# Performance work log

Measured on AMD Instinct MI355X. Metric: run time of the kernel, lower is better.

Reference implementation:

```python
import jax, jax.numpy as jnp
import numpy as np
import math

EMBED = 1024
HEADS = 16
HEAD_DIM = EMBED // HEADS
B, S = 4, 2048
FF = 4 * EMBED
EPS = 1e-5


def _layernorm(x, g, b):
    mu = jnp.mean(x, axis=-1, keepdims=True)
    var = jnp.mean(jnp.square(x - mu), axis=-1, keepdims=True)
    return (x - mu) * jax.lax.rsqrt(var + EPS) * g + b


def setup_inputs() -> dict:
    key = jax.random.key(0)
    ks = jax.random.split(key, 12)
    sd_e = 1.0 / math.sqrt(EMBED)
    sd_ff = 1.0 / math.sqrt(FF)
    return {
        "x": jax.random.normal(ks[0], (B, S, EMBED), jnp.float32),
        # attention weights stored [in, out] (transposed torch Linear)
        "Wq": jax.random.normal(ks[1], (EMBED, EMBED), jnp.float32) * sd_e,
        "bq": jnp.zeros((EMBED,), jnp.float32),
        "Wk": jax.random.normal(ks[2], (EMBED, EMBED), jnp.float32) * sd_e,
        "bk": jnp.zeros((EMBED,), jnp.float32),
        "Wv": jax.random.normal(ks[3], (EMBED, EMBED), jnp.float32) * sd_e,
        "bv": jnp.zeros((EMBED,), jnp.float32),
        "Wo": jax.random.normal(ks[4], (EMBED, EMBED), jnp.float32) * sd_e,
        "bo": jnp.zeros((EMBED,), jnp.float32),
        "g1": jnp.ones((EMBED,), jnp.float32),
        "beta1": jnp.zeros((EMBED,), jnp.float32),
        "g2": jnp.ones((EMBED,), jnp.float32),
        "beta2": jnp.zeros((EMBED,), jnp.float32),
        "W1": jax.random.normal(ks[5], (EMBED, FF), jnp.float32) * sd_e,
        "b1": jnp.zeros((FF,), jnp.float32),
        "W2": jax.random.normal(ks[6], (FF, EMBED), jnp.float32) * sd_ff,
        "b2": jnp.zeros((EMBED,), jnp.float32),
    }


def reference(x, Wq, bq, Wk, bk, Wv, bv, Wo, bo, g1, beta1, g2, beta2, W1, b1, W2, b2):
    b, s, _ = x.shape
    # --- pre-LN causal self-attention (dropout in eval = identity) ---
    h = _layernorm(x, g1, beta1)
    q = (h @ Wq + bq).reshape(b, s, HEADS, HEAD_DIM)
    k = (h @ Wk + bk).reshape(b, s, HEADS, HEAD_DIM)
    v = (h @ Wv + bv).reshape(b, s, HEADS, HEAD_DIM)
    scores = jnp.einsum("bqhd,bkhd->bhqk", q, k) / math.sqrt(HEAD_DIM)
    causal = jnp.tril(jnp.ones((s, s), bool))
    scores = jnp.where(causal, scores, jnp.float32(-1e8))
    attn = jax.nn.softmax(scores, axis=-1)
    y = jnp.einsum("bhqk,bkhd->bqhd", attn, v).reshape(b, s, EMBED)
    x = x + (y @ Wo + bo)
    # --- GELU MLP (exact erf gelu, torch default) ---
    h2 = _layernorm(x, g2, beta2)
    ff = jax.nn.gelu(h2 @ W1 + b1, approximate=False) @ W2 + b2
    return x + ff
```

## Files before the change

### kernel.cpp

```cpp
#include <hip/hip_runtime.h>
#include <hip/hip_bf16.h>
#include <stdint.h>
#include <math.h>

#define SEQ 2048
#define NTOK 8192
#define EMB 1024
#define NH 16
#define HD 64
#define FFD 4096

using us = unsigned short;
using b8 = __attribute__((ext_vector_type(8))) __bf16;
using f4 = __attribute__((ext_vector_type(4))) float;

__device__ __forceinline__ us f2b(float f) {
  union { float f; uint32_t u; } v; v.f = f;
  uint32_t u = v.u;
  return (us)((u + 0x7fffu + ((u >> 16) & 1u)) >> 16);
}

__device__ __forceinline__ uint32_t pkbf(float a, float b) {
  union { float f; uint32_t u; } x, y; x.f = a; y.f = b;
  return ((x.u + 0x8000u) >> 16) | ((y.u + 0x8000u) & 0xFFFF0000u);
}

__device__ __forceinline__ void async16(void* lds, const void* g) {
  __builtin_amdgcn_global_load_lds(
      (__attribute__((address_space(1))) void*)(uintptr_t)g,
      (__attribute__((address_space(3))) void*)(uintptr_t)lds, 16, 0, 0);
}

#define FENCED_BARRIER() do { asm volatile("" ::: "memory"); \
  __builtin_amdgcn_s_barrier(); asm volatile("" ::: "memory"); } while (0)

__device__ __forceinline__ float gelu_f(float x) {
  const float z = -2.30211416f * x * (1.f + 0.044715f * x * x);
  return x / (1.f + __builtin_amdgcn_exp2f(z));
}

__global__ __launch_bounds__(256)
void transpose_cast(const float* __restrict__ in, us* __restrict__ out, int R, int C) {
  __shared__ float tile[32][33];
  const int bc = blockIdx.x * 32, br = blockIdx.y * 32;
  const int tx = threadIdx.x & 31, ty = threadIdx.x >> 5;
#pragma unroll
  for (int i = 0; i < 32; i += 8)
    tile[ty + i][tx] = in[(size_t)(br + ty + i) * C + bc + tx];
  __syncthreads();
#pragma unroll
  for (int i = 0; i < 32; i += 8)
    out[(size_t)(bc + ty + i) * R + br + tx] = f2b(tile[tx][ty + i]);
}

__global__ void pack_bias(const float* __restrict__ bq, const float* __restrict__ bk,
                          const float* __restrict__ bv, float* __restrict__ o) {
  int i = blockIdx.x * 256 + threadIdx.x;
  o[i] = (i < 1024) ? bq[i] : (i < 2048 ? bk[i - 1024] : bv[i - 2048]);
}

__global__ __launch_bounds__(256)
void ln_kernel(const float* __restrict__ x, const float* __restrict__ g,
               const float* __restrict__ be, us* __restrict__ out) {
  __shared__ float red[8];
  const int row = blockIdx.x, t = threadIdx.x;
  const float4 v = ((const float4*)(x + (size_t)row * EMB))[t];
  float s = v.x + v.y + v.z + v.w;
  float s2 = v.x * v.x + v.y * v.y + v.z * v.z + v.w * v.w;
#pragma unroll
  for (int o = 32; o; o >>= 1) { s += __shfl_down(s, o, 64); s2 += __shfl_down(s2, o, 64); }
  if ((t & 63) == 0) { red[(t >> 6) * 2] = s; red[(t >> 6) * 2 + 1] = s2; }
  __syncthreads();
  const float ts = red[0] + red[2] + red[4] + red[6];
  const float ts2 = red[1] + red[3] + red[5] + red[7];
  const float mu = ts * (1.f / 1024.f);
  const float rs = rsqrtf(ts2 * (1.f / 1024.f) - mu * mu + 1e-5f);
  const float4 gv = ((const float4*)g)[t];
  const float4 bv = ((const float4*)be)[t];
  ushort4 o4;
  o4.x = f2b((v.x - mu) * rs * gv.x + bv.x);
  o4.y = f2b((v.y - mu) * rs * gv.y + bv.y);
  o4.z = f2b((v.z - mu) * rs * gv.z + bv.z);
  o4.w = f2b((v.w - mu) * rs * gv.w + bv.w);
  ((ushort4*)(out + (size_t)row * EMB))[t] = o4;
}

__global__ __launch_bounds__(512, 2)
void gemm256(const us* __restrict__ A, const us* __restrict__ Bt,
             const float* __restrict__ bias, us* __restrict__ outB,
             int N, int K, int gelu, int gy) {
  __shared__ us As[2][256 * 64];
  __shared__ us Bs[2][256 * 64];

  int bid = blockIdx.x;
  const int cpx = (int)gridDim.x >> 3;
  bid = (bid & 7) * cpx + (bid >> 3);
  const int bx = bid / gy, by = bid - bx * gy;
  const int row0 = bx * 256, col0 = by * 256;

  const int tid = threadIdx.x, w = tid >> 6, lane = tid & 63;
  const int wm = w >> 2, wn = w & 3;
  const int quad = lane >> 4, l15 = lane & 15;
  const int xr = l15 & 7;

  const int u0 = w * 2, u1 = u0 + 1;
  const int ar0 = ((u0 & 7) << 3) + ((u0 >> 3) << 7);
  const int ar1 = ((u1 & 7) << 3) + ((u1 >> 3) << 7);
  const int br0 = ((u0 & 3) << 3) + ((u0 >> 2) << 6);
  const int br1 = ((u1 & 3) << 3) + ((u1 >> 2) << 6);
  const int lrow = lane >> 3;
  const int loct = ((lane & 7) ^ lrow) << 3;
  const us* Ag0 = A + (size_t)(row0 + ar0 + lrow) * K + loct;
  const us* Ag1 = A + (size_t)(row0 + ar1 + lrow) * K + loct;
  const us* Bg0 = Bt + (size_t)(col0 + br0 + lrow) * K + loct;
  const us* Bg1 = Bt + (size_t)(col0 + br1 + lrow) * K + loct;
  const int NT = K >> 6;

  const f4 zf = {0.f, 0.f, 0.f, 0.f};
  f4 acc[8][4];
#pragma unroll
  for (int i = 0; i < 8; i++)
#pragma unroll
    for (int j = 0; j < 4; j++) acc[i][j] = zf;

  auto stgA = [&](int buf, int t, int mh) {
    const size_t go = (size_t)(mh << 6) * K + ((size_t)t << 6);
    async16(&As[buf][(ar0 + (mh << 6)) << 6], Ag0 + go);
    async16(&As[buf][(ar1 + (mh << 6)) << 6], Ag1 + go);
  };
  auto stgB = [&](int buf, int t, int nh) {
    const size_t go = (size_t)(nh << 5) * K + ((size_t)t << 6);
    async16(&Bs[buf][(br0 + (nh << 5)) << 6], Bg0 + go);
    async16(&Bs[buf][(br1 + (nh << 5)) << 6], Bg1 + go);
  };

  stgA(0, 0, 0); stgB(0, 0, 0); stgB(0, 0, 1); stgA(0, 0, 1);
  stgA(1, 1, 0); stgB(1, 1, 0); stgB(1, 1, 1);
  asm volatile("s_waitcnt vmcnt(6)" ::: "memory");
  FENCED_BARRIER();

  for (int t = 0; t < NT; t++) {
    const int cur = t & 1, nxt = cur ^ 1;
    const us* __restrict__ as = As[cur];
    const us* __restrict__ bs = Bs[cur];
    b8 af[2][4], bf0[2][2], bf1[2][2];

#pragma unroll
    for (int s = 0; s < 2; s++) {
      const int po = (((s << 2) + quad) ^ xr) << 3;
#pragma unroll
      for (int mi = 0; mi < 4; mi++)
        af[s][mi] = *(const b8*)&as[(wm * 128 + mi * 16 + l15) * 64 + po];
#pragma unroll
      for (int nf = 0; nf < 2; nf++)
        bf0[s][nf] = *(const b8*)&bs[(wn * 64 + nf * 16 + l15) * 64 + po];
    }
    if (t + 1 < NT) stgA(nxt, t + 1, 1);
    FENCED_BARRIER();
    asm volatile("s_waitcnt lgkmcnt(0)" ::: "memory");
    __builtin_amdgcn_s_setprio(1);
#pragma unroll
    for (int s = 0; s < 2; s++)
#pragma unroll
      for (int mi = 0; mi < 4; mi++)
#pragma unroll
        for (int nf = 0; nf < 2; nf++)
          acc[mi][nf] = __builtin_amdgcn_mfma_f32_16x16x32_bf16(af[s][mi], bf0[s][nf], acc[mi][nf], 0, 0, 0);
    __builtin_amdgcn_s_setprio(0);
    FENCED_BARRIER();

#pragma unroll
    for (int s = 0; s < 2; s++) {
      const int po = (((s << 2) + quad) ^ xr) << 3;
#pragma unroll
      for (int nf = 0; nf < 2; nf++)
        bf1[s][nf] = *(const b8*)&bs[(wn * 64 + 32 + nf * 16 + l15) * 64 + po];
    }
    if (t + 2 < NT) stgA(cur, t + 2, 0);
    FENCED_BARRIER();
    asm volatile("s_waitcnt lgkmcnt(0)" ::: "memory");
    __builtin_amdgcn_s_setprio(1);
#pragma unroll
    for (int s = 0; s < 2; s++)
#pragma unroll
      for (int mi = 0; mi < 4; mi++)
#pragma unroll
        for (int nf = 0; nf < 2; nf++)
          acc[mi][2 + nf] = __builtin_amdgcn_mfma_f32_16x16x32_bf16(af[s][mi], bf1[s][nf], acc[mi][2 + nf], 0, 0, 0);
    __builtin_amdgcn_s_setprio(0);
    FENCED_BARRIER();

#pragma unroll
    for (int s = 0; s < 2; s++) {
      const int po = (((s << 2) + quad) ^ xr) << 3;
#pragma unroll
      for (int mi = 0; mi < 4; mi++)
        af[s][mi] = *(const b8*)&as[(wm * 128 + 64 + mi * 16 + l15) * 64 + po];
    }
    if (t + 2 < NT) stgB(cur, t + 2, 0);
    FENCED_BARRIER();
    asm volatile("s_waitcnt lgkmcnt(0)" ::: "memory");
    __builtin_amdgcn_s_setprio(1);
#pragma unroll
    for (int s = 0; s < 2; s++)
#pragma unroll
      for (int mi = 0; mi < 4; mi++)
#pragma unroll
        for (int nf = 0; nf < 2; nf++)
          acc[4 + mi][nf] = __builtin_amdgcn_mfma_f32_16x16x32_bf16(af[s][mi], bf0[s][nf], acc[4 + mi][nf], 0, 0, 0);
    __builtin_amdgcn_s_setprio(0);
    FENCED_BARRIER();

    if (t + 2 < NT) {
      stgB(cur, t + 2, 1);
      asm volatile("s_waitcnt vmcnt(6)" ::: "memory");
    } else {
      asm volatile("s_waitcnt vmcnt(0)" ::: "memory");
    }
    FENCED_BARRIER();
    __builtin_amdgcn_s_setprio(1);
#pragma unroll
    for (int s = 0; s < 2; s++)
#pragma unroll
      for (int mi = 0; mi < 4; mi++)
#pragma unroll
        for (int nf = 0; nf < 2; nf++)
          acc[4 + mi][2 + nf] = __builtin_amdgcn_mfma_f32_16x16x32_bf16(af[s][mi], bf1[s][nf], acc[4 + mi][2 + nf], 0, 0, 0);
    __builtin_amdgcn_s_setprio(0);
    FENCED_BARRIER();
  }

#pragma unroll
  for (int mi8 = 0; mi8 < 8; mi8++)
#pragma unroll
    for (int nf = 0; nf < 4; nf++) {
      const int gcol = col0 + wn * 64 + nf * 16 + l15;
      const float bc = bias[gcol];
#pragma unroll
      for (int r = 0; r < 4; r++) {
        const int grow = row0 + wm * 128 + mi8 * 16 + quad * 4 + r;
        float v = acc[mi8][nf][r] + bc;
        if (gelu) v = gelu_f(v);
        outB[(size_t)grow * N + gcol] = f2b(v);
      }
    }
}

__global__ __launch_bounds__(512, 2)
void gemm128(const us* __restrict__ A, const us* __restrict__ Bt,
             const float* __restrict__ bias, const float* __restrict__ resid,
             float* __restrict__ outF, int N, int K, int gy) {
  __shared__ us As[2][128 * 64];
  __shared__ us Bs[2][256 * 64];

  int bid = blockIdx.x;
  const int cpx = (int)gridDim.x >> 3;
  bid = (bid & 7) * cpx + (bid >> 3);
  const int bx = bid / gy, by = bid - bx * gy;
  const int row0 = bx * 128, col0 = by * 256;

  const int tid = threadIdx.x, w = tid >> 6, lane = tid & 63;
  const int wm = w >> 2, wn = w & 3;
  const int quad = lane >> 4, l15 = lane & 15;
  const int xr = l15 & 7;

  const int u0 = w * 2, u1 = u0 + 1;
  const int aR0 = u0 << 3, aR1 = u1 << 3;
  const int bR0 = ((u0 & 3) << 3) + ((u0 >> 2) << 6);
  const int bR1 = ((u1 & 3) << 3) + ((u1 >> 2) << 6);
  const int lrow = lane >> 3;
  const int loct = ((lane & 7) ^ lrow) << 3;
  const us* Ag0 = A + (size_t)(row0 + aR0 + lrow) * K + loct;
  const us* Ag1 = A + (size_t)(row0 + aR1 + lrow) * K + loct;
  const us* Bg0 = Bt + (size_t)(col0 + bR0 + lrow) * K + loct;
  const us* Bg1 = Bt + (size_t)(col0 + bR1 + lrow) * K + loct;
  const int NT = K >> 6;

  const f4 zf = {0.f, 0.f, 0.f, 0.f};
  f4 acc[4][4];
#pragma unroll
  for (int i = 0; i < 4; i++)
#pragma unroll
    for (int j = 0; j < 4; j++) acc[i][j] = zf;

  auto stgA = [&](int buf, int t) {
    const size_t go = (size_t)t << 6;
    async16(&As[buf][aR0 << 6], Ag0 + go);
    async16(&As[buf][aR1 << 6], Ag1 + go);
  };
  auto stgB = [&](int buf, int t, int nh) {
    const size_t go = (size_t)(nh << 5) * K + ((size_t)t << 6);
    async16(&Bs[buf][(bR0 + (nh << 5)) << 6], Bg0 + go);
    async16(&Bs[buf][(bR1 + (nh << 5)) << 6], Bg1 + go);
  };

  stgA(0, 0); stgB(0, 0, 0); stgB(0, 0, 1);
  stgA(1, 1); stgB(1, 1, 0);
  asm volatile("s_waitcnt vmcnt(6)" ::: "memory");
  FENCED_BARRIER();

  for (int t = 0; t < NT; t++) {
    const int cur = t & 1, nxt = cur ^ 1;
    const us* __restrict__ as = As[cur];
    const us* __restrict__ bs = Bs[cur];
    b8 af[2][4], bf0[2][2], bf1[2][2];

#pragma unroll
    for (int s = 0; s < 2; s++) {
      const int po = (((s << 2) + quad) ^ xr) << 3;
#pragma unroll
      for (int mi = 0; mi < 4; mi++)
        af[s][mi] = *(const b8*)&as[(wm * 64 + mi * 16 + l15) * 64 + po];
#pragma unroll
      for (int nf = 0; nf < 2; nf++)
        bf0[s][nf] = *(const b8*)&bs[(wn * 64 + nf * 16 + l15) * 64 + po];
    }
    if (t + 1 < NT) {
      stgB(nxt, t + 1, 1);
      asm volatile("s_waitcnt vmcnt(6)" ::: "memory");
    } else {
      asm volatile("s_waitcnt vmcnt(0)" ::: "memory");
    }
    FENCED_BARRIER();
    asm volatile("s_waitcnt lgkmcnt(0)" ::: "memory");
    __builtin_amdgcn_s_setprio(1);
#pragma unroll
    for (int s = 0; s < 2; s++)
#pragma unroll
      for (int mi = 0; mi < 4; mi++)
#pragma unroll
        for (int nf = 0; nf < 2; nf++)
          acc[mi][nf] = __builtin_amdgcn_mfma_f32_16x16x32_bf16(af[s][mi], bf0[s][nf], acc[mi][nf], 0, 0, 0);
    __builtin_amdgcn_s_setprio(0);
    FENCED_BARRIER();

#pragma unroll
    for (int s = 0; s < 2; s++) {
      const int po = (((s << 2) + quad) ^ xr) << 3;
#pragma unroll
      for (int nf = 0; nf < 2; nf++)
        bf1[s][nf] = *(const b8*)&bs[(wn * 64 + 32 + nf * 16 + l15) * 64 + po];
    }
    if (t + 2 < NT) {
      stgA(cur, t + 2); stgB(cur, t + 2, 0);
      asm volatile("s_waitcnt vmcnt(6)" ::: "memory");
    } else {
      asm volatile("s_waitcnt vmcnt(2)" ::: "memory");
    }
    FENCED_BARRIER();
    asm volatile("s_waitcnt lgkmcnt(0)" ::: "memory");
    __builtin_amdgcn_s_setprio(1);
#pragma unroll
    for (int s = 0; s < 2; s++)
#pragma unroll
      for (int mi = 0; mi < 4; mi++)
#pragma unroll
        for (int nf = 0; nf < 2; nf++)
          acc[mi][2 + nf] = __builtin_amdgcn_mfma_f32_16x16x32_bf16(af[s][mi], bf1[s][nf], acc[mi][2 + nf], 0, 0, 0);
    __builtin_amdgcn_s_setprio(0);
    FENCED_BARRIER();
  }

#pragma unroll
  for (int mi = 0; mi < 4; mi++)
#pragma unroll
    for (int nf = 0; nf < 4; nf++) {
      const int gcol = col0 + wn * 64 + nf * 16 + l15;
      const float bc = bias[gcol];
#pragma unroll
      for (int r = 0; r < 4; r++) {
        const int grow = row0 + wm * 64 + mi * 16 + quad * 4 + r;
        outF[(size_t)grow * N + gcol] = acc[mi][nf][r] + bc + resid[(size_t)grow * N + gcol];
      }
    }
}

__global__ __launch_bounds__(256, 3)
void attn(const us* __restrict__ qkv, us* __restrict__ y) {
  static const signed char QTM[16] = {15,14,13,12, 10,11,8,9, 5,4,7,6, 0,1,2,3};
  const int bx = blockIdx.x;
  const int bh = bx & 63;
  const int qt = QTM[(bx >> 6) & 15];
  const int bb = bh >> 4, h = bh & 15;
  const int tid = threadIdx.x;
  const int wave = tid >> 6, lane = tid & 63;
  const int quad = lane >> 4, l15 = lane & 15;

  __shared__ us Ks[128 * 64];
  __shared__ us Vt[64 * 132];

  const size_t base = (size_t)bb * SEQ * 3072;
  const int q0 = qt * 128;

  b8 bqf[2][2];
#pragma unroll
  for (int qg = 0; qg < 2; qg++) {
    const us* qp = qkv + base + (size_t)(q0 + wave * 32 + qg * 16 + l15) * 3072 + h * 64 + quad * 8;
    bqf[qg][0] = *(const b8*)qp;
    bqf[qg][1] = *(const b8*)(qp + 32);
  }

  const f4 zf = {0.f, 0.f, 0.f, 0.f};
  f4 o[2][4];
  float mrow[2], lrow[2];
#pragma unroll
  for (int qg = 0; qg < 2; qg++) {
    mrow[qg] = -3.0e38f; lrow[qg] = 0.f;
#pragma unroll
    for (int dg = 0; dg < 4; dg++) o[qg][dg] = zf;
  }

  const int klr = lane >> 3, klc = lane & 7;
  const us* kgbase = qkv + base + (size_t)(wave * 32 + klr) * 3072 + 1024 + h * 64 + ((klc ^ klr) << 3);
  const us* vgbase = qkv + base + (size_t)(2 * lane) * 3072 + 2048 + h * 64 + wave * 8;

  const float sm_scale = 0.125f * 1.44269504088896340736f;

  for (int kt = 0; kt <= qt; kt++) {
    const size_t koff = (size_t)kt * 128 * 3072;
#pragma unroll
    for (int op = 0; op < 4; op++)
      async16(&Ks[(wave * 32 + op * 8) * 64], kgbase + koff + (size_t)op * 8 * 3072);
    {
      union { float4 f; us u[8]; } v0, v1, v2, v3;
      v0.f = *(const float4*)(vgbase + koff);
      v1.f = *(const float4*)(vgbase + koff + 3072);
      v2.f = *(const float4*)(vgbase + koff + 32);
      v3.f = *(const float4*)(vgbase + koff + 3072 + 32);
#pragma unroll
      for (int j = 0; j < 8; j++) {
        *(uint32_t*)&Vt[(wave * 8 + j) * 132 + 2 * lane] =
            (uint32_t)v0.u[j] | ((uint32_t)v1.u[j] << 16);
        *(uint32_t*)&Vt[(32 + wave * 8 + j) * 132 + 2 * lane] =
            (uint32_t)v2.u[j] | ((uint32_t)v3.u[j] << 16);
      }
    }
    __syncthreads();

    f4 sacc[2][8];
#pragma unroll
    for (int c = 0; c < 8; c++) {
      const int krow = (c * 16 + l15) * 64;
      const int sw = l15 & 7;
      const b8 ak0 = *(const b8*)&Ks[krow + ((quad ^ sw) << 3)];
      const b8 ak1 = *(const b8*)&Ks[krow + (((quad ^ 4) ^ sw) << 3)];
#pragma unroll
      for (int qg = 0; qg < 2; qg++) {
        f4 s = __builtin_amdgcn_mfma_f32_16x16x32_bf16(ak0, bqf[qg][0], zf, 0, 0, 0);
        sacc[qg][c] = __builtin_amdgcn_mfma_f32_16x16x32_bf16(ak1, bqf[qg][1], s, 0, 0, 0);
      }
    }

    uint32_t pf[2][16];
    float alpha[2];
#pragma unroll
    for (int qg = 0; qg < 2; qg++) {
      const int q_in = wave * 32 + qg * 16 + l15;
#pragma unroll
      for (int c = 0; c < 8; c++)
#pragma unroll
        for (int r = 0; r < 4; r++) {
          float v = sacc[qg][c][r] * sm_scale;
          if (kt == qt && (c * 16 + quad * 4 + r) > q_in) v = -3.0e38f;
          sacc[qg][c][r] = v;
        }
      float mx = sacc[qg][0][0];
#pragma unroll
      for (int c = 0; c < 8; c++)
#pragma unroll
        for (int r = 0; r < 4; r++) mx = fmaxf(mx, sacc[qg][c][r]);
      mx = fmaxf(mx, __shfl_xor(mx, 16, 64));
      mx = fmaxf(mx, __shfl_xor(mx, 32, 64));
      const float mnew = fmaxf(mrow[qg], mx);
      alpha[qg] = __builtin_amdgcn_exp2f(mrow[qg] - mnew);
      mrow[qg] = mnew;
      float rs = 0.f;
#pragma unroll
      for (int c = 0; c < 8; c++) {
        const float p0 = __builtin_amdgcn_exp2f(sacc[qg][c][0] - mnew);
        const float p1 = __builtin_amdgcn_exp2f(sacc[qg][c][1] - mnew);
        const float p2 = __builtin_amdgcn_exp2f(sacc[qg][c][2] - mnew);
        const float p3 = __builtin_amdgcn_exp2f(sacc[qg][c][3] - mnew);
        rs += (p0 + p1) + (p2 + p3);
        pf[qg][c * 2] = pkbf(p0, p1);
        pf[qg][c * 2 + 1] = pkbf(p2, p3);
      }
      rs += __shfl_xor(rs, 16, 64);
      rs += __shfl_xor(rs, 32, 64);
      lrow[qg] = lrow[qg] * alpha[qg] + rs;
#pragma unroll
      for (int r = 0; r < 4; r++) {
        const float ar = __shfl(alpha[qg], quad * 4 + r, 64);
#pragma unroll
        for (int dg = 0; dg < 4; dg++) o[qg][dg][r] *= ar;
      }
    }

#pragma unroll
    for (int c = 0; c < 8; c++) {
      union { uint32_t w[4]; b8 v; } af0, af1;
      af0.w[0] = pf[0][c * 2]; af0.w[1] = pf[0][c * 2 + 1]; af0.w[2] = 0u; af0.w[3] = 0u;
      af1.w[0] = pf[1][c * 2]; af1.w[1] = pf[1][c * 2 + 1]; af1.w[2] = 0u; af1.w[3] = 0u;
#pragma unroll
      for (int dg = 0; dg < 4; dg++) {
        const uint2 vd = *(const uint2*)&Vt[(dg * 16 + l15) * 132 + c * 16 + quad * 4];
        union { uint32_t w[4]; b8 v; } vb;
        vb.w[0] = vd.x; vb.w[1] = vd.y; vb.w[2] = 0u; vb.w[3] = 0u;
        o[0][dg] = __builtin_amdgcn_mfma_f32_16x16x32_bf16(af0.v, vb.v, o[0][dg], 0, 0, 0);
        o[1][dg] = __builtin_amdgcn_mfma_f32_16x16x32_bf16(af1.v, vb.v, o[1][dg], 0, 0, 0);
      }
    }
    __syncthreads();
  }

#pragma unroll
  for (int qg = 0; qg < 2; qg++) {
    float lr[4];
#pragma unroll
    for (int r = 0; r < 4; r++) lr[r] = __shfl(lrow[qg], quad * 4 + r, 64);
#pragma unroll
    for (int dg = 0; dg < 4; dg++)
#pragma unroll
      for (int r = 0; r < 4; r++) {
        const int gq = q0 + wave * 32 + qg * 16 + quad * 4 + r;
        y[(size_t)(bb * SEQ + gq) * EMB + h * 64 + dg * 16 + l15] = f2b(o[qg][dg][r] / lr[r]);
      }
  }
}

extern "C" void kernel_launch(void* const* d_in, const int* in_sizes, int n_in,
                              void* d_out, int out_size, void* d_ws, size_t ws_size,
                              hipStream_t stream) {
  const float* x = (const float*)d_in[0];
  const float* Wq = (const float*)d_in[1];
  const float* bq = (const float*)d_in[2];
  const float* Wk = (const float*)d_in[3];
  const float* bk = (const float*)d_in[4];
  const float* Wv = (const float*)d_in[5];
  const float* bv = (const float*)d_in[6];
  const float* Wo = (const float*)d_in[7];
  const float* bo = (const float*)d_in[8];
  const float* g1 = (const float*)d_in[9];
  const float* be1 = (const float*)d_in[10];
  const float* g2 = (const float*)d_in[11];
  const float* be2 = (const float*)d_in[12];
  const float* W1 = (const float*)d_in[13];
  const float* b1 = (const float*)d_in[14];
  const float* W2 = (const float*)d_in[15];
  const float* b2 = (const float*)d_in[16];
  float* out = (float*)d_out;

  char* ws = (char*)d_ws;
  const size_t MB = 1024ull * 1024ull;
  us* WqkvT = (us*)(ws + 0);
  us* WoT   = (us*)(ws + 6 * MB);
  us* W1T   = (us*)(ws + 8 * MB);
  us* W2T   = (us*)(ws + 16 * MB);
  us* hbuf  = (us*)(ws + 24 * MB);
  us* qkvb  = (us*)(ws + 40 * MB);
  us* ybuf  = (us*)(ws + 88 * MB);
  float* x1 = (float*)(ws + 104 * MB);
  us* h2    = (us*)(ws + 136 * MB);
  us* ff1   = (us*)(ws + 24 * MB);
  float* bqkv = (float*)(ws + 152 * MB);

  transpose_cast<<<dim3(32, 32), 256, 0, stream>>>(Wq, WqkvT, 1024, 1024);
  transpose_cast<<<dim3(32, 32), 256, 0, stream>>>(Wk, WqkvT + 1024 * 1024, 1024, 1024);
  transpose_cast<<<dim3(32, 32), 256, 0, stream>>>(Wv, WqkvT + 2 * 1024 * 1024, 1024, 1024);
  transpose_cast<<<dim3(32, 32), 256, 0, stream>>>(Wo, WoT, 1024, 1024);
  transpose_cast<<<dim3(128, 32), 256, 0, stream>>>(W1, W1T, 1024, 4096);
  transpose_cast<<<dim3(32, 128), 256, 0, stream>>>(W2, W2T, 4096, 1024);
  pack_bias<<<12, 256, 0, stream>>>(bq, bk, bv, bqkv);

  ln_kernel<<<NTOK, 256, 0, stream>>>(x, g1, be1, hbuf);
  gemm256<<<dim3(384), 512, 0, stream>>>(hbuf, WqkvT, bqkv, qkvb, 3072, 1024, 0, 12);
  attn<<<1024, 256, 0, stream>>>(qkvb, ybuf);
  gemm128<<<dim3(256), 512, 0, stream>>>(ybuf, WoT, bo, x, x1, 1024, 1024, 4);
  ln_kernel<<<NTOK, 256, 0, stream>>>(x1, g2, be2, h2);
  gemm256<<<dim3(512), 512, 0, stream>>>(h2, W1T, b1, ff1, 4096, 1024, 1, 16);
  gemm128<<<dim3(256), 512, 0, stream>>>(ff1, W2T, b2, x1, out, 1024, 4096, 4);
}
```

Baseline: 540.8 us.

## Fold softmax scale into Wq, prefetch V, lazy rescale in attention

Folds the 1/sqrt(d)·log2(e) softmax scale into the Wq weights and q bias during the weight cast, so the per-element scale multiply leaves the attention loop. The next V tile is now prefetched into registers while the current tile is computed, with explicit waitcnt and barriers. Online-softmax rescaling is skipped unless the running max grows by more than 8 (in log2 units), and s_setprio is raised around the MFMA sections. Occupancy hint goes from 3 to 4 blocks per CU, which constrains registers even though the prefetch needs more of them. The lazy rescale allows unnormalized values up to 2^8, and scaling Wq before the bf16 cast changes rounding slightly.

After: 628.1 us. 1.16x slower.

```diff
diff --git a/kernel.cpp b/kernel.cpp
--- a/kernel.cpp
+++ b/kernel.cpp
@@ -9,6 +9,7 @@
 #define NH 16
 #define HD 64
 #define FFD 4096
+#define QSCALE 0.1803368801111137f
 
 using us = unsigned short;
 using b8 = __attribute__((ext_vector_type(8))) __bf16;
@@ -40,7 +41,8 @@
 }
 
 __global__ __launch_bounds__(256)
-void transpose_cast(const float* __restrict__ in, us* __restrict__ out, int R, int C) {
+void transpose_cast(const float* __restrict__ in, us* __restrict__ out, int R, int C,
+                    float scale) {
   __shared__ float tile[32][33];
   const int bc = blockIdx.x * 32, br = blockIdx.y * 32;
   const int tx = threadIdx.x & 31, ty = threadIdx.x >> 5;
@@ -50,13 +52,13 @@
   __syncthreads();
 #pragma unroll
   for (int i = 0; i < 32; i += 8)
-    out[(size_t)(bc + ty + i) * R + br + tx] = f2b(tile[tx][ty + i]);
+    out[(size_t)(bc + ty + i) * R + br + tx] = f2b(tile[tx][ty + i] * scale);
 }
 
 __global__ void pack_bias(const float* __restrict__ bq, const float* __restrict__ bk,
                           const float* __restrict__ bv, float* __restrict__ o) {
   int i = blockIdx.x * 256 + threadIdx.x;
-  o[i] = (i < 1024) ? bq[i] : (i < 2048 ? bk[i - 1024] : bv[i - 2048]);
+  o[i] = (i < 1024) ? bq[i] * QSCALE : (i < 2048 ? bk[i - 1024] : bv[i - 2048]);
 }
 
 __global__ __launch_bounds__(256)
@@ -375,7 +377,7 @@
     }
 }
 
-__global__ __launch_bounds__(256, 3)
+__global__ __launch_bounds__(256, 4)
 void attn(const us* __restrict__ qkv, us* __restrict__ y) {
   static const signed char QTM[16] = {15,14,13,12, 10,11,8,9, 5,4,7,6, 0,1,2,3};
   const int bx = blockIdx.x;
@@ -414,7 +416,10 @@
   const us* kgbase = qkv + base + (size_t)(wave * 32 + klr) * 3072 + 1024 + h * 64 + ((klc ^ klr) << 3);
   const us* vgbase = qkv + base + (size_t)(2 * lane) * 3072 + 2048 + h * 64 + wave * 8;
 
-  const float sm_scale = 0.125f * 1.44269504088896340736f;
+  float4 va0 = *(const float4*)(vgbase);
+  float4 va1 = *(const float4*)(vgbase + 3072);
+  float4 va2 = *(const float4*)(vgbase + 32);
+  float4 va3 = *(const float4*)(vgbase + 3072 + 32);
 
   for (int kt = 0; kt <= qt; kt++) {
     const size_t koff = (size_t)kt * 128 * 3072;
@@ -423,10 +428,7 @@
       async16(&Ks[(wave * 32 + op * 8) * 64], kgbase + koff + (size_t)op * 8 * 3072);
     {
       union { float4 f; us u[8]; } v0, v1, v2, v3;
-      v0.f = *(const float4*)(vgbase + koff);
-      v1.f = *(const float4*)(vgbase + koff + 3072);
-      v2.f = *(const float4*)(vgbase + koff + 32);
-      v3.f = *(const float4*)(vgbase + koff + 3072 + 32);
+      v0.f = va0; v1.f = va1; v2.f = va2; v3.f = va3;
 #pragma unroll
       for (int j = 0; j < 8; j++) {
         *(uint32_t*)&Vt[(wave * 8 + j) * 132 + 2 * lane] =
@@ -435,9 +437,22 @@
             (uint32_t)v2.u[j] | ((uint32_t)v3.u[j] << 16);
       }
     }
-    __syncthreads();
+    float4 vb0, vb1, vb2, vb3;
+    if (kt < qt) {
+      const us* vg = vgbase + koff + (size_t)128 * 3072;
+      vb0 = *(const float4*)(vg);
+      vb1 = *(const float4*)(vg + 3072);
+      vb2 = *(const float4*)(vg + 32);
+      vb3 = *(const float4*)(vg + 3072 + 32);
+      asm volatile("s_waitcnt vmcnt(4)" ::: "memory");
+    } else {
+      asm volatile("s_waitcnt vmcnt(0)" ::: "memory");
+    }
+    asm volatile("s_waitcnt lgkmcnt(0)" ::: "memory");
+    FENCED_BARRIER();
 
     f4 sacc[2][8];
+    __builtin_amdgcn_s_setprio(1);
 #pragma unroll
     for (int c = 0; c < 8; c++) {
       const int krow = (c * 16 + l15) * 64;
@@ -450,20 +465,19 @@
         sacc[qg][c] = __builtin_amdgcn_mfma_f32_16x16x32_bf16(ak1, bqf[qg][1], s, 0, 0, 0);
       }
     }
+    __builtin_amdgcn_s_setprio(0);
 
     uint32_t pf[2][16];
-    float alpha[2];
 #pragma unroll
     for (int qg = 0; qg < 2; qg++) {
       const int q_in = wave * 32 + qg * 16 + l15;
-#pragma unroll
-      for (int c = 0; c < 8; c++)
-#pragma unroll
-        for (int r = 0; r < 4; r++) {
-          float v = sacc[qg][c][r] * sm_scale;
-          if (kt == qt && (c * 16 + quad * 4 + r) > q_in) v = -3.0e38f;
-          sacc[qg][c][r] = v;
-        }
+      if (kt == qt) {
+#pragma unroll
+        for (int c = 0; c < 8; c++)
+#pragma unroll
+          for (int r = 0; r < 4; r++)
+            if ((c * 16 + quad * 4 + r) > q_in) sacc[qg][c][r] = -3.0e38f;
+      }
       float mx = sacc[qg][0][0];
 #pragma unroll
       for (int c = 0; c < 8; c++)
@@ -471,31 +485,36 @@
         for (int r = 0; r < 4; r++) mx = fmaxf(mx, sacc[qg][c][r]);
       mx = fmaxf(mx, __shfl_xor(mx, 16, 64));
       mx = fmaxf(mx, __shfl_xor(mx, 32, 64));
-      const float mnew = fmaxf(mrow[qg], mx);
-      alpha[qg] = __builtin_amdgcn_exp2f(mrow[qg] - mnew);
-      mrow[qg] = mnew;
+      if (!__all(mx - mrow[qg] <= 8.f)) {
+        const float mnew = fmaxf(mrow[qg], mx);
+        const float al = __builtin_amdgcn_exp2f(mrow[qg] - mnew);
+        mrow[qg] = mnew;
+        lrow[qg] *= al;
+#pragma unroll
+        for (int r = 0; r < 4; r++) {
+          const float ar = __shfl(al, quad * 4 + r, 64);
+#pragma unroll
+          for (int dg = 0; dg < 4; dg++) o[qg][dg][r] *= ar;
+        }
+      }
+      const float mb = mrow[qg];
       float rs = 0.f;
 #pragma unroll
       for (int c = 0; c < 8; c++) {
-        const float p0 = __builtin_amdgcn_exp2f(sacc[qg][c][0] - mnew);
-        const float p1 = __builtin_amdgcn_exp2f(sacc[qg][c][1] - mnew);
-        const float p2 = __builtin_amdgcn_exp2f(sacc[qg][c][2] - mnew);
-        const float p3 = __builtin_amdgcn_exp2f(sacc[qg][c][3] - mnew);
+        const float p0 = __builtin_amdgcn_exp2f(sacc[qg][c][0] - mb);
+        const float p1 = __builtin_amdgcn_exp2f(sacc[qg][c][1] - mb);
+        const float p2 = __builtin_amdgcn_exp2f(sacc[qg][c][2] - mb);
+        const float p3 = __builtin_amdgcn_exp2f(sacc[qg][c][3] - mb);
         rs += (p0 + p1) + (p2 + p3);
         pf[qg][c * 2] = pkbf(p0, p1);
         pf[qg][c * 2 + 1] = pkbf(p2, p3);
       }
       rs += __shfl_xor(rs, 16, 64);
       rs += __shfl_xor(rs, 32, 64);
-      lrow[qg] = lrow[qg] * alpha[qg] + rs;
-#pragma unroll
-      for (int r = 0; r < 4; r++) {
-        const float ar = __shfl(alpha[qg], quad * 4 + r, 64);
-#pragma unroll
-        for (int dg = 0; dg < 4; dg++) o[qg][dg][r] *= ar;
-      }
-    }
-
+      lrow[qg] += rs;
+    }
+
+    __builtin_amdgcn_s_setprio(1);
 #pragma unroll
     for (int c = 0; c < 8; c++) {
       union { uint32_t w[4]; b8 v; } af0, af1;
@@ -510,7 +529,12 @@
         o[1][dg] = __builtin_amdgcn_mfma_f32_16x16x32_bf16(af1.v, vb.v, o[1][dg], 0, 0, 0);
       }
     }
-    __syncthreads();
+    __builtin_amdgcn_s_setprio(0);
+    asm volatile("s_waitcnt lgkmcnt(0)" ::: "memory");
+    FENCED_BARRIER();
+    if (kt < qt) {
+      va0 = vb0; va1 = vb1; va2 = vb2; va3 = vb3;
+    }
   }
 
 #pragma unroll
@@ -564,12 +588,12 @@
   us* ff1   = (us*)(ws + 24 * MB);
   float* bqkv = (float*)(ws + 152 * MB);
 
-  transpose_cast<<<dim3(32, 32), 256, 0, stream>>>(Wq, WqkvT, 1024, 1024);
-  transpose_cast<<<dim3(32, 32), 256, 0, stream>>>(Wk, WqkvT + 1024 * 1024, 1024, 1024);
-  transpose_cast<<<dim3(32, 32), 256, 0, stream>>>(Wv, WqkvT + 2 * 1024 * 1024, 1024, 1024);
-  transpose_cast<<<dim3(32, 32), 256, 0, stream>>>(Wo, WoT, 1024, 1024);
-  transpose_cast<<<dim3(128, 32), 256, 0, stream>>>(W1, W1T, 1024, 4096);
-  transpose_cast<<<dim3(32, 128), 256, 0, stream>>>(W2, W2T, 4096, 1024);
+  transpose_cast<<<dim3(32, 32), 256, 0, stream>>>(Wq, WqkvT, 1024, 1024, QSCALE);
+  transpose_cast<<<dim3(32, 32), 256, 0, stream>>>(Wk, WqkvT + 1024 * 1024, 1024, 1024, 1.f);
+  transpose_cast<<<dim3(32, 32), 256, 0, stream>>>(Wv, WqkvT + 2 * 1024 * 1024, 1024, 1024, 1.f);
+  transpose_cast<<<dim3(32, 32), 256, 0, stream>>>(Wo, WoT, 1024, 1024, 1.f);
+  transpose_cast<<<dim3(128, 32), 256, 0, stream>>>(W1, W1T, 1024, 4096, 1.f);
+  transpose_cast<<<dim3(32, 128), 256, 0, stream>>>(W2, W2T, 4096, 1024, 1.f);
   pack_bias<<<12, 256, 0, stream>>>(bq, bk, bv, bqkv);
 
   ln_kernel<<<NTOK, 256, 0, stream>>>(x, g1, be1, hbuf);
```
